# Kernel tuning notes

Hardware: AMD Instinct MI355X
Metric: run time of the kernel (lower is better)

The kernel has to match this reference:

```python
import jax, jax.numpy as jnp
import numpy as np

EMBED_DIM = 1024
NUM_HEADS = 16
HEAD_DIM = EMBED_DIM // NUM_HEADS
SCALE = 1.0 / np.sqrt(HEAD_DIM).astype(np.float32)


def setup_inputs() -> dict:
    key = jax.random.key(0)
    ks = jax.random.split(key, 9)
    B, T, C = 2, 2048, EMBED_DIM
    s = 1.0 / np.sqrt(C).astype(np.float32)  # torch Linear init scale (approx, uniform bound)
    return {
        "x_q": jax.random.normal(ks[0], (B, T, C), dtype=jnp.float32),
        "attn_mask": jnp.zeros((T, T), dtype=jnp.float32),
        "Wq": jax.random.uniform(ks[1], (C, C), jnp.float32, -s, s),
        "bq": jax.random.uniform(ks[2], (C,), jnp.float32, -s, s),
        "Wk": jax.random.uniform(ks[3], (C, C), jnp.float32, -s, s),
        "bk": jax.random.uniform(ks[4], (C,), jnp.float32, -s, s),
        "Wv": jax.random.uniform(ks[5], (C, C), jnp.float32, -s, s),
        "bv": jax.random.uniform(ks[6], (C,), jnp.float32, -s, s),
        "Wo": jax.random.uniform(ks[7], (C, C), jnp.float32, -s, s),
        "bo": jax.random.uniform(ks[8], (C,), jnp.float32, -s, s),
    }


def reference(x_q, attn_mask, Wq, bq, Wk, bk, Wv, bv, Wo, bo):
    B, Tq, C = x_q.shape
    # self-attention: x_kv = x_q
    q = (x_q @ Wq.T + bq).reshape(B, Tq, NUM_HEADS, HEAD_DIM)
    k = (x_q @ Wk.T + bk).reshape(B, Tq, NUM_HEADS, HEAD_DIM)
    v = (x_q @ Wv.T + bv).reshape(B, Tq, NUM_HEADS, HEAD_DIM)
    # (B, H, Tq, Tk)
    scores = jnp.einsum('bqhd,bkhd->bhqk', q, k) * SCALE
    scores = scores + attn_mask[None, None, :, :]  # 2D additive mask path
    attn = jax.nn.softmax(scores, axis=-1)  # dropout p=0.0 -> identity
    out = jnp.einsum('bhqk,bkhd->bqhd', attn, v).reshape(B, Tq, C)
    out = out @ Wo.T + bo
    return out
```

## Files before the change

### kernel.cpp

```cpp
#include <hip/hip_runtime.h>
#include <hip/hip_bf16.h>
#include <stdint.h>

typedef _Float16 f16x8_t __attribute__((ext_vector_type(8)));
typedef _Float16 f16x4_t __attribute__((ext_vector_type(4)));
typedef float    f32x4_t __attribute__((ext_vector_type(4)));

#define T_SEQ 2048
#define NH    16
#define HD    64
#define CDIM  1024
#define NTOK  4096
#define QSCALE 0.18033688011112042f
#define LOG2E  1.4426950408889634f

__device__ __forceinline__ void async_ld16(void* lds, const void* g) {
    __builtin_amdgcn_global_load_lds(
        (const __attribute__((address_space(1))) uint32_t*)g,
        (__attribute__((address_space(3))) uint32_t*)lds, 16, 0, 0);
}

__global__ __launch_bounds__(256)
void prep_all(const float* __restrict__ x, const float* __restrict__ Wq,
              const float* __restrict__ Wk, const float* __restrict__ Wv,
              const float* __restrict__ Wo, const float* __restrict__ mask,
              _Float16* __restrict__ xh, _Float16* __restrict__ Wqkvh,
              _Float16* __restrict__ Woh, int* __restrict__ flag)
{
    const int XQ = NTOK * CDIM / 4;
    const int WQ = CDIM * CDIM / 4;
    int i = blockIdx.x * 256 + threadIdx.x;
    if (i < XQ + 4 * WQ) {
        const float* s; _Float16* d; int off;
        if (i < XQ) { s = x; d = xh; off = i; }
        else {
            int j = i - XQ; int w = j >> 18; off = j & (WQ - 1);
            s = (w == 0) ? Wq : (w == 1) ? Wk : (w == 2) ? Wv : Wo;
            d = (w == 3) ? Woh : Wqkvh + (size_t)w * CDIM * CDIM;
        }
        float4 v = ((const float4*)s)[off];
        f16x4_t h = {(_Float16)v.x, (_Float16)v.y, (_Float16)v.z, (_Float16)v.w};
        ((f16x4_t*)d)[off] = h;
    } else {
        int off = i - (XQ + 4 * WQ);
        float4 v = ((const float4*)mask)[off];
        if (v.x != 0.f || v.y != 0.f || v.z != 0.f || v.w != 0.f) atomicOr(flag, 1);
    }
}

template<int MODE>
__global__ __launch_bounds__(256)
void gemm_f16(const _Float16* __restrict__ Ag, const _Float16* __restrict__ Bg,
              const float* __restrict__ b0, const float* __restrict__ b1,
              const float* __restrict__ b2,
              _Float16* __restrict__ Qo, _Float16* __restrict__ Ko,
              _Float16* __restrict__ Vto, float* __restrict__ Fo)
{
    __shared__ _Float16 sA[2][128 * 32];
    __shared__ _Float16 sB[2][128 * 32];
    const int K = CDIM;
    const int tid  = threadIdx.x;
    const int lane = tid & 63, wv = tid >> 6;
    const int wr = wv >> 1, wc = wv & 1;
    const int rowA0 = blockIdx.x * 128;
    const int rowB0 = blockIdx.y * 128;
    const int srow = lane >> 2;
    const int scol = (lane & 3) * 8;
    const int fr = lane & 15, fg = lane >> 4;
    f32x4_t acc[4][4] = {};

#define STAGE(buf, kk) do {                                                     \
        _Pragma("unroll")                                                       \
        for (int i_ = 0; i_ < 2; ++i_) {                                        \
            const int eoff = i_ * 2048 + wv * 512;                              \
            const int r_ = i_ * 64 + wv * 16 + srow;                            \
            async_ld16(&sA[buf][eoff], Ag + (size_t)(rowA0 + r_) * K + (kk) + scol); \
            async_ld16(&sB[buf][eoff], Bg + (size_t)(rowB0 + r_) * K + (kk) + scol); \
        } } while (0)

    STAGE(0, 0);
    for (int k0 = 0; k0 < K; k0 += 32) {
        const int cur = (k0 >> 5) & 1;
        __syncthreads();
        if (k0 + 32 < K) STAGE(cur ^ 1, k0 + 32);
        f16x8_t a[4], b[4];
#pragma unroll
        for (int mi = 0; mi < 4; ++mi)
            a[mi] = *(const f16x8_t*)&sA[cur][(wr * 64 + mi * 16 + fr) * 32 + fg * 8];
#pragma unroll
        for (int ni = 0; ni < 4; ++ni)
            b[ni] = *(const f16x8_t*)&sB[cur][(wc * 64 + ni * 16 + fr) * 32 + fg * 8];
#pragma unroll
        for (int mi = 0; mi < 4; ++mi)
#pragma unroll
            for (int ni = 0; ni < 4; ++ni)
                acc[mi][ni] = __builtin_amdgcn_mfma_f32_16x16x32_f16(a[mi], b[ni], acc[mi][ni], 0, 0, 0);
    }
#undef STAGE

#pragma unroll
    for (int mi = 0; mi < 4; ++mi) {
#pragma unroll
        for (int ni = 0; ni < 4; ++ni) {
            const int col = rowB0 + wc * 64 + ni * 16 + fr;
#pragma unroll
            for (int r = 0; r < 4; ++r) {
                const int row = rowA0 + wr * 64 + mi * 16 + fg * 4 + r;
                float v = acc[mi][ni][r];
                if (MODE == 0) {
                    const int which = col >> 10, cc = col & 1023;
                    const float* bp = (which == 0) ? b0 : ((which == 1) ? b1 : b2);
                    v += bp[cc];
                    const int bb = row >> 11, tt = row & (T_SEQ - 1);
                    const int h = cc >> 6, d = cc & 63;
                    const int bh = bb * NH + h;
                    const size_t tbase = ((size_t)bh * 32 + (tt >> 6)) * 4096;
                    if (which == 0)
                        Qo[((size_t)bh * T_SEQ + tt) * HD + d] = (_Float16)(v * QSCALE);
                    else if (which == 1)
                        Ko[tbase + (size_t)(d >> 3) * 512 + (tt & 63) * 8 + (d & 7)] = (_Float16)v;
                    else
                        Vto[tbase + (size_t)((tt >> 3) & 7) * 512 + d * 8 + (tt & 7)] = (_Float16)v;
                } else {
                    Fo[(size_t)row * CDIM + col] = v + b0[col];
                }
            }
        }
    }
}

__global__ __launch_bounds__(512, 4)
void attn_f16(const _Float16* __restrict__ Q, const _Float16* __restrict__ Kc,
              const _Float16* __restrict__ Vc, const float* __restrict__ mask,
              const int* __restrict__ mflag, _Float16* __restrict__ AO)
{
    __shared__ __align__(16) _Float16 sK[2][4096];
    __shared__ __align__(16) _Float16 sV[2][4096];
    __shared__ __align__(16) _Float16 Ps[8][1024];

    const int tid = threadIdx.x;
    const int lane = tid & 63, wv = tid >> 6;
    const int fr = lane & 15, fg = lane >> 4;
    const int bh = blockIdx.y;
    const int b = bh >> 4, h = bh & (NH - 1);
    const int q0 = blockIdx.x * 128 + wv * 16;
    const _Float16* Qb  = Q  + (size_t)bh * T_SEQ * HD;
    const _Float16* Kbh = Kc + (size_t)bh * (T_SEQ * HD);
    const _Float16* Vbh = Vc + (size_t)bh * (T_SEQ * HD);
    const int soff = wv * 512 + lane * 8;

    f16x8_t qf[2];
#pragma unroll
    for (int dc = 0; dc < 2; ++dc)
        qf[dc] = *(const f16x8_t*)&Qb[(size_t)(q0 + fr) * HD + dc * 32 + fg * 8];

    f32x4_t o[4] = {};
    float m_run = -1e30f, l_run = 0.f;
    const int mf = mflag[0];

    async_ld16(&sK[0][wv * 512], Kbh + soff);
    async_ld16(&sV[0][wv * 512], Vbh + soff);

    for (int t = 0; t < T_SEQ / 64; ++t) {
        const int cur = t & 1;
        __syncthreads();
        if (t + 1 < T_SEQ / 64) {
            async_ld16(&sK[cur ^ 1][wv * 512], Kbh + (t + 1) * 4096 + soff);
            async_ld16(&sV[cur ^ 1][wv * 512], Vbh + (t + 1) * 4096 + soff);
        }

        f32x4_t s[4];
        __builtin_amdgcn_s_setprio(1);
#pragma unroll
        for (int kt = 0; kt < 4; ++kt) {
            f16x8_t kf0 = *(const f16x8_t*)&sK[cur][fg * 512       + (kt * 16 + fr) * 8];
            f16x8_t kf1 = *(const f16x8_t*)&sK[cur][(4 + fg) * 512 + (kt * 16 + fr) * 8];
            f32x4_t z = {};
            z     = __builtin_amdgcn_mfma_f32_16x16x32_f16(kf0, qf[0], z, 0, 0, 0);
            s[kt] = __builtin_amdgcn_mfma_f32_16x16x32_f16(kf1, qf[1], z, 0, 0, 0);
        }
        __builtin_amdgcn_s_setprio(0);

        f16x8_t vb[2][4];
#pragma unroll
        for (int kt2 = 0; kt2 < 2; ++kt2)
#pragma unroll
            for (int df = 0; df < 4; ++df)
                vb[kt2][df] = *(const f16x8_t*)&sV[cur][(kt2 * 4 + fg) * 512 + (df * 16 + fr) * 8];

        if (mf) {
            const float* mrow = mask + (size_t)(q0 + fr) * T_SEQ + t * 64;
#pragma unroll
            for (int kt = 0; kt < 4; ++kt)
#pragma unroll
                for (int r = 0; r < 4; ++r)
                    s[kt][r] += mrow[kt * 16 + fg * 4 + r] * LOG2E;
        }

        float tmax = -1e30f;
#pragma unroll
        for (int kt = 0; kt < 4; ++kt)
            tmax = fmaxf(tmax, fmaxf(fmaxf(s[kt][0], s[kt][1]), fmaxf(s[kt][2], s[kt][3])));
        tmax = fmaxf(tmax, __shfl_xor(tmax, 16, 64));
        tmax = fmaxf(tmax, __shfl_xor(tmax, 32, 64));

        if (!__all(tmax <= m_run + 8.0f)) {
            const float mnew = fmaxf(m_run, tmax);
            const float sc = __builtin_amdgcn_exp2f(m_run - mnew);
            m_run = mnew;
            float scq[4];
#pragma unroll
            for (int r = 0; r < 4; ++r)
                scq[r] = __shfl(sc, fg * 4 + r, 64);
#pragma unroll
            for (int df = 0; df < 4; ++df)
#pragma unroll
                for (int r = 0; r < 4; ++r)
                    o[df][r] *= scq[r];
            l_run *= sc;
        }

        float rs = 0.f;
#pragma unroll
        for (int kt = 0; kt < 4; ++kt) {
            f16x4_t hp;
#pragma unroll
            for (int r = 0; r < 4; ++r) {
                const float p = __builtin_amdgcn_exp2f(s[kt][r] - m_run);
                rs += p;
                hp[r] = (_Float16)p;
            }
            *(f16x4_t*)&Ps[wv][(kt * 2 + (fg >> 1)) * 128 + fr * 8 + (fg & 1) * 4] = hp;
        }
        rs += __shfl_xor(rs, 16, 64);
        rs += __shfl_xor(rs, 32, 64);
        l_run += rs;

        asm volatile("s_waitcnt lgkmcnt(0)" ::: "memory");
        __builtin_amdgcn_sched_barrier(0);

        __builtin_amdgcn_s_setprio(1);
#pragma unroll
        for (int kt2 = 0; kt2 < 2; ++kt2) {
            f16x8_t pa = *(const f16x8_t*)&Ps[wv][(kt2 * 4 + fg) * 128 + fr * 8];
#pragma unroll
            for (int df = 0; df < 4; ++df)
                o[df] = __builtin_amdgcn_mfma_f32_16x16x32_f16(pa, vb[kt2][df], o[df], 0, 0, 0);
        }
        __builtin_amdgcn_s_setprio(0);
    }

    float lq[4];
#pragma unroll
    for (int r = 0; r < 4; ++r)
        lq[r] = __shfl(l_run, fg * 4 + r, 64);
#pragma unroll
    for (int r = 0; r < 4; ++r) {
        const float inv = 1.f / lq[r];
        const size_t row = (size_t)(b * T_SEQ + q0 + fg * 4 + r);
#pragma unroll
        for (int df = 0; df < 4; ++df)
            AO[row * CDIM + h * HD + df * 16 + fr] = (_Float16)(o[df][r] * inv);
    }
}

extern "C" void kernel_launch(void* const* d_in, const int* in_sizes, int n_in,
                              void* d_out, int out_size, void* d_ws, size_t ws_size,
                              hipStream_t stream) {
    const float* x    = (const float*)d_in[0];
    const float* mask = (const float*)d_in[1];
    const float* Wq   = (const float*)d_in[2];
    const float* bq   = (const float*)d_in[3];
    const float* Wk   = (const float*)d_in[4];
    const float* bk   = (const float*)d_in[5];
    const float* Wv   = (const float*)d_in[6];
    const float* bv   = (const float*)d_in[7];
    const float* Wo   = (const float*)d_in[8];
    const float* bo   = (const float*)d_in[9];
    float* out = (float*)d_out;

    char* ws = (char*)d_ws;
    _Float16* xh    = (_Float16*)(ws);
    _Float16* Wqkvh = (_Float16*)(ws + (8u  << 20));
    _Float16* Woh   = (_Float16*)(ws + (14u << 20));
    _Float16* Qp    = (_Float16*)(ws + (16u << 20));
    _Float16* Kc    = (_Float16*)(ws + (24u << 20));
    _Float16* Vc    = (_Float16*)(ws + (32u << 20));
    int* mflag      = (int*)(ws + (40u << 20));
    _Float16* AO    = xh;

    hipMemsetAsync(mflag, 0, 4, stream);
    prep_all<<<12288, 256, 0, stream>>>(x, Wq, Wk, Wv, Wo, mask, xh, Wqkvh, Woh, mflag);
    gemm_f16<0><<<dim3(32, 24), 256, 0, stream>>>(xh, Wqkvh, bq, bk, bv,
                                                  Qp, Kc, Vc, nullptr);
    attn_f16<<<dim3(16, 32), 512, 0, stream>>>(Qp, Kc, Vc, mask, mflag, AO);
    gemm_f16<1><<<dim3(32, 8), 256, 0, stream>>>(AO, Woh, bo, nullptr, nullptr,
                                                 nullptr, nullptr, nullptr, out);
}
```

Before: 134.4 us.

## Swap GEMM operands, swizzle workgroup order, vectorize epilogue, compute rowsum via MFMA

The GEMMs now take the weights as operand A and the activations as operand B, so each lane's four accumulator rows are contiguous output columns. That lets the epilogue load bias as a float4 and store f16x4 or float4 vectors instead of scalars. Both the GEMM and attention kernels move to a 1D grid with an XCD-style block swizzle, aimed at better L2 locality across the chiplets. In attention, the softmax row sum is now accumulated by an extra MFMA against a ones vector, replacing the per-tile shuffle reductions; this adds MFMA work but removes cross-lane sums. The max reduction is also rebalanced into a flatter tree.

```diff
diff --git a/kernel.cpp b/kernel.cpp
--- a/kernel.cpp
+++ b/kernel.cpp
@@ -59,11 +59,15 @@
     __shared__ _Float16 sA[2][128 * 32];
     __shared__ _Float16 sB[2][128 * 32];
     const int K = CDIM;
+    const int NBX = (MODE == 0) ? 24 : 8;
+    const int NWG = NBX * 32;
     const int tid  = threadIdx.x;
     const int lane = tid & 63, wv = tid >> 6;
     const int wr = wv >> 1, wc = wv & 1;
-    const int rowA0 = blockIdx.x * 128;
-    const int rowB0 = blockIdx.y * 128;
+    const int bid = blockIdx.x;
+    const int swz = (bid & 7) * (NWG / 8) + (bid >> 3);
+    const int rowA0 = (swz % NBX) * 128;
+    const int rowB0 = (swz / NBX) * 128;
     const int srow = lane >> 2;
     const int scol = (lane & 3) * 8;
     const int fr = lane & 15, fg = lane >> 4;
@@ -98,32 +102,49 @@
     }
 #undef STAGE
 
-#pragma unroll
-    for (int mi = 0; mi < 4; ++mi) {
-#pragma unroll
-        for (int ni = 0; ni < 4; ++ni) {
-            const int col = rowB0 + wc * 64 + ni * 16 + fr;
-#pragma unroll
-            for (int r = 0; r < 4; ++r) {
-                const int row = rowA0 + wr * 64 + mi * 16 + fg * 4 + r;
-                float v = acc[mi][ni][r];
-                if (MODE == 0) {
-                    const int which = col >> 10, cc = col & 1023;
-                    const float* bp = (which == 0) ? b0 : ((which == 1) ? b1 : b2);
-                    v += bp[cc];
-                    const int bb = row >> 11, tt = row & (T_SEQ - 1);
-                    const int h = cc >> 6, d = cc & 63;
-                    const int bh = bb * NH + h;
-                    const size_t tbase = ((size_t)bh * 32 + (tt >> 6)) * 4096;
-                    if (which == 0)
-                        Qo[((size_t)bh * T_SEQ + tt) * HD + d] = (_Float16)(v * QSCALE);
-                    else if (which == 1)
-                        Ko[tbase + (size_t)(d >> 3) * 512 + (tt & 63) * 8 + (d & 7)] = (_Float16)v;
-                    else
-                        Vto[tbase + (size_t)((tt >> 3) & 7) * 512 + d * 8 + (tt & 7)] = (_Float16)v;
+    if (MODE == 0) {
+        const int which = rowA0 >> 10;
+        const float* bp = (which == 0) ? b0 : ((which == 1) ? b1 : b2);
+#pragma unroll
+        for (int mi = 0; mi < 4; ++mi) {
+            const int cc = (rowA0 & 1023) + wr * 64 + mi * 16 + fg * 4;
+            const float4 bv = *(const float4*)&bp[cc];
+            const int h = cc >> 6, d0 = cc & 63;
+#pragma unroll
+            for (int ni = 0; ni < 4; ++ni) {
+                const int tok = rowB0 + wc * 64 + ni * 16 + fr;
+                const int bh = (tok >> 11) * NH + h, tt = tok & (T_SEQ - 1);
+                const float v0 = acc[mi][ni][0] + bv.x, v1 = acc[mi][ni][1] + bv.y;
+                const float v2 = acc[mi][ni][2] + bv.z, v3 = acc[mi][ni][3] + bv.w;
+                if (which == 0) {
+                    f16x4_t hq = {(_Float16)(v0 * QSCALE), (_Float16)(v1 * QSCALE),
+                                  (_Float16)(v2 * QSCALE), (_Float16)(v3 * QSCALE)};
+                    *(f16x4_t*)&Qo[((size_t)bh * T_SEQ + tt) * HD + d0] = hq;
+                } else if (which == 1) {
+                    f16x4_t hk = {(_Float16)v0, (_Float16)v1, (_Float16)v2, (_Float16)v3};
+                    *(f16x4_t*)&Ko[((size_t)bh * 32 + (tt >> 6)) * 4096 +
+                                   (d0 >> 3) * 512 + (tt & 63) * 8 + (d0 & 7)] = hk;
                 } else {
-                    Fo[(size_t)row * CDIM + col] = v + b0[col];
+                    const size_t vb_ = ((size_t)bh * 32 + (tt >> 6)) * 4096 +
+                                       (size_t)((tt >> 3) & 7) * 512 + (tt & 7);
+                    Vto[vb_ + (d0 + 0) * 8] = (_Float16)v0;
+                    Vto[vb_ + (d0 + 1) * 8] = (_Float16)v1;
+                    Vto[vb_ + (d0 + 2) * 8] = (_Float16)v2;
+                    Vto[vb_ + (d0 + 3) * 8] = (_Float16)v3;
                 }
+            }
+        }
+    } else {
+#pragma unroll
+        for (int mi = 0; mi < 4; ++mi) {
+            const int cc = rowA0 + wr * 64 + mi * 16 + fg * 4;
+            const float4 bv = *(const float4*)&b0[cc];
+#pragma unroll
+            for (int ni = 0; ni < 4; ++ni) {
+                const int tok = rowB0 + wc * 64 + ni * 16 + fr;
+                float4 ov = {acc[mi][ni][0] + bv.x, acc[mi][ni][1] + bv.y,
+                             acc[mi][ni][2] + bv.z, acc[mi][ni][3] + bv.w};
+                *(float4*)&Fo[(size_t)tok * CDIM + cc] = ov;
             }
         }
     }
@@ -141,9 +162,11 @@
     const int tid = threadIdx.x;
     const int lane = tid & 63, wv = tid >> 6;
     const int fr = lane & 15, fg = lane >> 4;
-    const int bh = blockIdx.y;
+    const int bid = blockIdx.x;
+    const int swz = (bid & 7) * 64 + (bid >> 3);
+    const int qx = swz & 15, bh = swz >> 4;
     const int b = bh >> 4, h = bh & (NH - 1);
-    const int q0 = blockIdx.x * 128 + wv * 16;
+    const int q0 = qx * 128 + wv * 16;
     const _Float16* Qb  = Q  + (size_t)bh * T_SEQ * HD;
     const _Float16* Kbh = Kc + (size_t)bh * (T_SEQ * HD);
     const _Float16* Vbh = Vc + (size_t)bh * (T_SEQ * HD);
@@ -154,8 +177,11 @@
     for (int dc = 0; dc < 2; ++dc)
         qf[dc] = *(const f16x8_t*)&Qb[(size_t)(q0 + fr) * HD + dc * 32 + fg * 8];
 
+    const f16x8_t ones = {(_Float16)1.f, (_Float16)1.f, (_Float16)1.f, (_Float16)1.f,
+                          (_Float16)1.f, (_Float16)1.f, (_Float16)1.f, (_Float16)1.f};
     f32x4_t o[4] = {};
-    float m_run = -1e30f, l_run = 0.f;
+    f32x4_t lacc = {};
+    float m_run = -1e30f;
     const int mf = mflag[0];
 
     async_ld16(&sK[0][wv * 512], Kbh + soff);
@@ -197,10 +223,12 @@
                     s[kt][r] += mrow[kt * 16 + fg * 4 + r] * LOG2E;
         }
 
-        float tmax = -1e30f;
-#pragma unroll
-        for (int kt = 0; kt < 4; ++kt)
-            tmax = fmaxf(tmax, fmaxf(fmaxf(s[kt][0], s[kt][1]), fmaxf(s[kt][2], s[kt][3])));
+        const float t0 = fmaxf(fmaxf(s[0][0], s[0][1]), s[0][2]);
+        const float t1 = fmaxf(fmaxf(s[0][3], s[1][0]), s[1][1]);
+        const float t2 = fmaxf(fmaxf(s[1][2], s[1][3]), s[2][0]);
+        const float t3 = fmaxf(fmaxf(s[2][1], s[2][2]), s[2][3]);
+        const float t4 = fmaxf(fmaxf(s[3][0], s[3][1]), s[3][2]);
+        float tmax = fmaxf(fmaxf(fmaxf(t0, t1), fmaxf(t2, t3)), fmaxf(t4, s[3][3]));
         tmax = fmaxf(tmax, __shfl_xor(tmax, 16, 64));
         tmax = fmaxf(tmax, __shfl_xor(tmax, 32, 64));
 
@@ -213,28 +241,22 @@
             for (int r = 0; r < 4; ++r)
                 scq[r] = __shfl(sc, fg * 4 + r, 64);
 #pragma unroll
-            for (int df = 0; df < 4; ++df)
-#pragma unroll
-                for (int r = 0; r < 4; ++r)
+            for (int r = 0; r < 4; ++r) {
+                lacc[r] *= scq[r];
+#pragma unroll
+                for (int df = 0; df < 4; ++df)
                     o[df][r] *= scq[r];
-            l_run *= sc;
-        }
-
-        float rs = 0.f;
+            }
+        }
+
 #pragma unroll
         for (int kt = 0; kt < 4; ++kt) {
             f16x4_t hp;
 #pragma unroll
-            for (int r = 0; r < 4; ++r) {
-                const float p = __builtin_amdgcn_exp2f(s[kt][r] - m_run);
-                rs += p;
-                hp[r] = (_Float16)p;
-            }
+            for (int r = 0; r < 4; ++r)
+                hp[r] = (_Float16)__builtin_amdgcn_exp2f(s[kt][r] - m_run);
             *(f16x4_t*)&Ps[wv][(kt * 2 + (fg >> 1)) * 128 + fr * 8 + (fg & 1) * 4] = hp;
         }
-        rs += __shfl_xor(rs, 16, 64);
-        rs += __shfl_xor(rs, 32, 64);
-        l_run += rs;
 
         asm volatile("s_waitcnt lgkmcnt(0)" ::: "memory");
         __builtin_amdgcn_sched_barrier(0);
@@ -246,17 +268,14 @@
 #pragma unroll
             for (int df = 0; df < 4; ++df)
                 o[df] = __builtin_amdgcn_mfma_f32_16x16x32_f16(pa, vb[kt2][df], o[df], 0, 0, 0);
+            lacc = __builtin_amdgcn_mfma_f32_16x16x32_f16(pa, ones, lacc, 0, 0, 0);
         }
         __builtin_amdgcn_s_setprio(0);
     }
 
-    float lq[4];
-#pragma unroll
-    for (int r = 0; r < 4; ++r)
-        lq[r] = __shfl(l_run, fg * 4 + r, 64);
 #pragma unroll
     for (int r = 0; r < 4; ++r) {
-        const float inv = 1.f / lq[r];
+        const float inv = 1.f / lacc[r];
         const size_t row = (size_t)(b * T_SEQ + q0 + fg * 4 + r);
 #pragma unroll
         for (int df = 0; df < 4; ++df)
@@ -291,9 +310,8 @@
 
     hipMemsetAsync(mflag, 0, 4, stream);
     prep_all<<<12288, 256, 0, stream>>>(x, Wq, Wk, Wv, Wo, mask, xh, Wqkvh, Woh, mflag);
-    gemm_f16<0><<<dim3(32, 24), 256, 0, stream>>>(xh, Wqkvh, bq, bk, bv,
-                                                  Qp, Kc, Vc, nullptr);
-    attn_f16<<<dim3(16, 32), 512, 0, stream>>>(Qp, Kc, Vc, mask, mflag, AO);
-    gemm_f16<1><<<dim3(32, 8), 256, 0, stream>>>(AO, Woh, bo, nullptr, nullptr,
-                                                 nullptr, nullptr, nullptr, out);
-}
+    gemm_f16<0><<<768, 256, 0, stream>>>(Wqkvh, xh, bq, bk, bv, Qp, Kc, Vc, nullptr);
+    attn_f16<<<512, 512, 0, stream>>>(Qp, Kc, Vc, mask, mflag, AO);
+    gemm_f16<1><<<256, 256, 0, stream>>>(Woh, AO, bo, nullptr, nullptr,
+                                         nullptr, nullptr, nullptr, out);
+}
```

Result: faster. 128.5 us (-4.4%).
